# Kernel tuning notes

Hardware: AMD Instinct MI355X
Metric: run time of the kernel (lower is better)

Reference implementation:

```python
import jax, jax.numpy as jnp
import numpy as np

N_HEAD, D_HEAD, D_MODEL = 16, 64, 1024
QLEN, MLEN, BSZ = 512, 512, 8
KLEN = QLEN + MLEN
SCALE = 1.0 / D_HEAD ** 0.5
LN_EPS = 1e-5


def rel_shift(x):
    # x: [qlen, klen, bsz, n_head] -- Transformer-XL pad/reshape shift trick
    q, k, b, n = x.shape
    x_pad = jnp.pad(x, ((0, 0), (1, 0), (0, 0), (0, 0)))
    x_pad = x_pad.reshape(k + 1, q, b, n)
    return x_pad[1:].reshape(q, k, b, n)


def setup_inputs() -> dict:
    key = jax.random.key(0)
    ks = jax.random.split(key, 10)
    s = 0.02
    return {
        'w': jax.random.normal(ks[0], (QLEN, BSZ, D_MODEL), jnp.float32),
        'r': jax.random.normal(ks[1], (KLEN, D_MODEL), jnp.float32),
        'mems': jax.random.normal(ks[2], (MLEN, BSZ, D_MODEL), jnp.float32),
        'r_w_bias': jax.random.normal(ks[3], (N_HEAD, D_HEAD), jnp.float32) * s,
        'r_r_bias': jax.random.normal(ks[4], (N_HEAD, D_HEAD), jnp.float32) * s,
        'Wq': jax.random.normal(ks[5], (N_HEAD * D_HEAD, D_MODEL), jnp.float32) * s,
        'Wkv': jax.random.normal(ks[6], (2 * N_HEAD * D_HEAD, D_MODEL), jnp.float32) * s,
        'Wr': jax.random.normal(ks[7], (N_HEAD * D_HEAD, D_MODEL), jnp.float32) * s,
        'br': jnp.zeros((N_HEAD * D_HEAD,), jnp.float32),
        'Wo': jax.random.normal(ks[8], (D_MODEL, N_HEAD * D_HEAD), jnp.float32) * s,
        'bo': jnp.zeros((D_MODEL,), jnp.float32),
        'gamma': jnp.ones((D_MODEL,), jnp.float32),
        'beta': jnp.zeros((D_MODEL,), jnp.float32),
    }


def reference(w, r, mems, r_w_bias, r_r_bias, Wq, Wkv, Wr, br, Wo, bo, gamma, beta):
    qlen, bsz, _ = w.shape
    cat = jnp.concatenate([mems, w], axis=0)           # [klen, b, d]
    klen = cat.shape[0]
    mlen = klen - qlen

    q = (w @ Wq.T).reshape(qlen, bsz, N_HEAD, D_HEAD)   # [i, b, n, d]
    kv = (cat @ Wkv.T).reshape(klen, bsz, N_HEAD, 2 * D_HEAD)
    k, v = kv[..., :D_HEAD], kv[..., D_HEAD:]           # [j, b, n, d]
    rk = (r @ Wr.T + br).reshape(klen, N_HEAD, D_HEAD)  # [j, n, d]

    AC = jnp.einsum('ibnd,jbnd->ijbn', q + r_w_bias, k)
    BD = jnp.einsum('ibnd,jnd->ijbn', q + r_r_bias, rk)
    BD = rel_shift(BD)
    score = (AC + BD) * SCALE                           # [i, j, b, n]

    # causal mask with memory: query i attends to keys j <= i + mlen
    i_idx = jnp.arange(qlen)[:, None]
    j_idx = jnp.arange(klen)[None, :]
    mask = j_idx > (i_idx + mlen)
    score = jnp.where(mask[:, :, None, None], -1e30, score)

    prob = jax.nn.softmax(score, axis=1)
    attn_vec = jnp.einsum('ijbn,jbnd->ibnd', prob, v).reshape(qlen, bsz, N_HEAD * D_HEAD)
    attn_out = attn_vec @ Wo.T + bo

    # IdentityResidualGate: x + relu(y), then LayerNorm
    y = w + jax.nn.relu(attn_out)
    mu = jnp.mean(y, axis=-1, keepdims=True)
    var = jnp.mean(jnp.square(y - mu), axis=-1, keepdims=True)
    return (y - mu) * jax.lax.rsqrt(var + LN_EPS) * gamma + beta
```

## Files before the change

kernel.cpp:

```cpp
#include <hip/hip_runtime.h>
#include <hip/hip_bf16.h>
#include <cstdint>
#include <cstddef>

typedef __attribute__((ext_vector_type(4))) float f32x4;
typedef __attribute__((ext_vector_type(8))) short bf16x8;
using u16 = unsigned short;

#define SCLOG2E 0.18033688011112043f

__device__ __forceinline__ u16 f2b(float f) {
    union { float f; uint32_t u; } x; x.f = f;
    uint32_t r = x.u + 0x7fffu + ((x.u >> 16) & 1u);
    return (u16)(r >> 16);
}
__device__ __forceinline__ float b2f(u16 u) {
    union { uint32_t u; float f; } x; x.u = (uint32_t)u << 16; return x.f;
}

#define GLDS16(g, s)                                                        \
    __builtin_amdgcn_global_load_lds(                                       \
        (const __attribute__((address_space(1))) uint32_t*)(g),             \
        (__attribute__((address_space(3))) uint32_t*)(s), 16, 0, 0)

__global__ __launch_bounds__(256) void prep_kernel(
    const float* __restrict__ mems, const float* __restrict__ w,
    const float* __restrict__ r, const float* __restrict__ Wq,
    const float* __restrict__ Wkv, const float* __restrict__ Wr,
    const float* __restrict__ Wo, u16* __restrict__ cat_b,
    u16* __restrict__ r_b, u16* __restrict__ Wq_b, u16* __restrict__ Wkv_b,
    u16* __restrict__ Wr_b, u16* __restrict__ Wo_b) {
    int bid = blockIdx.x;
    if (bid < 8192) {
        int col4 = threadIdx.x;
        float4 v;
        int b, oj;
        if (bid < 4096) {
            v = reinterpret_cast<const float4*>(mems)[(size_t)bid * 256 + col4];
            b = bid & 7; oj = bid >> 3;
        } else {
            int rrow = bid - 4096;
            v = reinterpret_cast<const float4*>(w)[(size_t)rrow * 256 + col4];
            b = rrow & 7; oj = 512 + (rrow >> 3);
        }
        uint2 o;
        o.x = (uint32_t)f2b(v.x) | ((uint32_t)f2b(v.y) << 16);
        o.y = (uint32_t)f2b(v.z) | ((uint32_t)f2b(v.w) << 16);
        reinterpret_cast<uint2*>(cat_b)[(size_t)(b * 1024 + oj) * 256 + col4] = o;
        return;
    }
    bid -= 8192;
    const float4* src;
    uint2* dst;
    if (bid < 1024)      { src = (const float4*)r;   dst = (uint2*)r_b; }
    else if (bid < 2048) { src = (const float4*)Wq;  dst = (uint2*)Wq_b;  bid -= 1024; }
    else if (bid < 4096) { src = (const float4*)Wkv; dst = (uint2*)Wkv_b; bid -= 2048; }
    else if (bid < 5120) { src = (const float4*)Wr;  dst = (uint2*)Wr_b;  bid -= 4096; }
    else                 { src = (const float4*)Wo;  dst = (uint2*)Wo_b;  bid -= 5120; }
    int idx = bid * 256 + threadIdx.x;
    float4 v = src[idx];
    uint2 o;
    o.x = (uint32_t)f2b(v.x) | ((uint32_t)f2b(v.y) << 16);
    o.y = (uint32_t)f2b(v.z) | ((uint32_t)f2b(v.w) << 16);
    dst[idx] = o;
}

__global__ __launch_bounds__(512, 1) void kv_gemm(const u16* __restrict__ catb,
                                                  const u16* __restrict__ Wkvb,
                                                  u16* __restrict__ kb,
                                                  u16* __restrict__ vtb) {
    __shared__ u16 sA[2][256][64];
    __shared__ u16 sB[2][256][64];
    const int tid = threadIdx.x;
    const int wid = tid >> 6, lane = tid & 63;
    const int lr = lane & 15, lg = lane >> 4;
    const int bm = blockIdx.x * 256, bn = blockIdx.y * 256;
    const int Wm = (wid >> 2) * 128, Wn = (wid & 3) * 64;
    const int srow = tid >> 3, scol = tid & 7;
    const int xs = lr & 7;
    const u16* A = catb + (size_t)bm * 1024;
    const u16* B = Wkvb + (size_t)bn * 1024;
    f32x4 acc[8][4] = {};

#pragma unroll
    for (int p = 0; p < 4; p++) {
        int row = p * 64 + srow;
        int cs = (scol ^ (row & 7)) * 8;
        GLDS16(A + (size_t)row * 1024 + cs, &sA[0][row][scol * 8]);
        GLDS16(B + (size_t)row * 1024 + cs, &sB[0][row][scol * 8]);
    }
    __syncthreads();

    int cur = 0;
    for (int t = 0; t < 16; t++) {
        if (t < 15) {
            const int k0n = (t + 1) * 64;
#pragma unroll
            for (int p = 0; p < 4; p++) {
                int row = p * 64 + srow;
                int cs = (scol ^ (row & 7)) * 8;
                GLDS16(A + (size_t)row * 1024 + k0n + cs, &sA[cur ^ 1][row][scol * 8]);
                GLDS16(B + (size_t)row * 1024 + k0n + cs, &sB[cur ^ 1][row][scol * 8]);
            }
        }
#pragma unroll
        for (int ks = 0; ks < 2; ks++) {
            bf16x8 af[8], bfr[4];
#pragma unroll
            for (int mi = 0; mi < 8; mi++)
                af[mi] = *reinterpret_cast<const bf16x8*>(
                    &sA[cur][Wm + mi * 16 + lr][((ks * 4 + lg) ^ xs) * 8]);
#pragma unroll
            for (int ni = 0; ni < 4; ni++)
                bfr[ni] = *reinterpret_cast<const bf16x8*>(
                    &sB[cur][Wn + ni * 16 + lr][((ks * 4 + lg) ^ xs) * 8]);
#pragma unroll
            for (int mi = 0; mi < 8; mi++)
#pragma unroll
                for (int ni = 0; ni < 4; ni++)
                    acc[mi][ni] = __builtin_amdgcn_mfma_f32_16x16x32_bf16(
                        af[mi], bfr[ni], acc[mi][ni], 0, 0, 0);
        }
        __syncthreads();
        cur ^= 1;
    }
#pragma unroll
    for (int mi = 0; mi < 8; mi++)
#pragma unroll
        for (int ni = 0; ni < 4; ni++) {
            const int m0 = bm + Wm + mi * 16 + lg * 4;
            const int c = bn + Wn + ni * 16 + lr;
            const int b = m0 >> 10, j0 = m0 & 1023;
            const int n = c >> 7, dd = c & 127;
            if (dd < 64) {
#pragma unroll
                for (int rr = 0; rr < 4; rr++)
                    kb[(((size_t)(b * 16 + n)) * 1024 + j0 + rr) * 64 + dd] =
                        f2b(acc[mi][ni][rr]);
            } else {
                uint2 pk;
                pk.x = (uint32_t)f2b(acc[mi][ni][0]) | ((uint32_t)f2b(acc[mi][ni][1]) << 16);
                pk.y = (uint32_t)f2b(acc[mi][ni][2]) | ((uint32_t)f2b(acc[mi][ni][3]) << 16);
                *reinterpret_cast<uint2*>(
                    vtb + (((size_t)(b * 16 + n)) * 64 + (dd - 64)) * 1024 + j0) = pk;
            }
        }
}

__global__ __launch_bounds__(256, 2) void qr_gemm(
    const u16* __restrict__ catb, const u16* __restrict__ Wqb,
    const u16* __restrict__ rb, const u16* __restrict__ Wrb,
    const float* __restrict__ bw, const float* __restrict__ brr,
    const float* __restrict__ br, u16* __restrict__ qwb,
    u16* __restrict__ qrb, u16* __restrict__ rkb) {
    __shared__ u16 sA[2][128][64];
    __shared__ u16 sB[2][128][64];
    const int idx = blockIdx.x;
    const u16 *A, *B;
    int bx, by, epi;
    if (idx < 256) {
        epi = 0; B = Wqb; bx = idx & 31; by = idx >> 5;
        int bm0 = bx * 128;
        A = catb + ((size_t)(bm0 >> 9) * 1024 + 512 + (bm0 & 511)) * 1024;
    } else {
        epi = 2; B = Wrb;
        int l = idx - 256; bx = l & 7; by = l >> 3;
        A = rb + (size_t)bx * 128 * 1024;
    }
    const int tid = threadIdx.x;
    const int wid = tid >> 6, lane = tid & 63;
    const int lr = lane & 15, lg = lane >> 4;
    const int bm = bx * 128, bn = by * 128;
    const int wm = (wid >> 1) * 64, wn = (wid & 1) * 64;
    const int srow = tid >> 3, scol = tid & 7;
    f32x4 acc[4][4] = {};

#pragma unroll
    for (int p = 0; p < 4; p++) {
        int row = p * 32 + srow;
        GLDS16(A + (size_t)row * 1024 + scol * 8, &sA[0][row][scol * 8]);
        GLDS16(B + (size_t)(bn + row) * 1024 + scol * 8, &sB[0][row][scol * 8]);
    }
    __syncthreads();

    int cur = 0;
    for (int t = 0; t < 16; t++) {
        if (t < 15) {
            const int k0n = (t + 1) * 64;
#pragma unroll
            for (int p = 0; p < 4; p++) {
                int row = p * 32 + srow;
                GLDS16(A + (size_t)row * 1024 + k0n + scol * 8, &sA[cur ^ 1][row][scol * 8]);
                GLDS16(B + (size_t)(bn + row) * 1024 + k0n + scol * 8,
                       &sB[cur ^ 1][row][scol * 8]);
            }
        }
#pragma unroll
        for (int ks = 0; ks < 2; ks++) {
            bf16x8 af[4], bfr[4];
#pragma unroll
            for (int x = 0; x < 4; x++) {
                af[x] = *reinterpret_cast<const bf16x8*>(
                    &sA[cur][wm + x * 16 + lr][(ks * 4 + lg) * 8]);
                bfr[x] = *reinterpret_cast<const bf16x8*>(
                    &sB[cur][wn + x * 16 + lr][(ks * 4 + lg) * 8]);
            }
#pragma unroll
            for (int mi = 0; mi < 4; mi++)
#pragma unroll
                for (int ni = 0; ni < 4; ni++)
                    acc[mi][ni] = __builtin_amdgcn_mfma_f32_16x16x32_bf16(
                        af[mi], bfr[ni], acc[mi][ni], 0, 0, 0);
        }
        __syncthreads();
        cur ^= 1;
    }
#pragma unroll
    for (int mi = 0; mi < 4; mi++)
#pragma unroll
        for (int ni = 0; ni < 4; ni++) {
            const int m0 = bm + wm + mi * 16 + lg * 4;
            const int c = bn + wn + ni * 16 + lr;
            if (epi == 0) {
#pragma unroll
                for (int rr = 0; rr < 4; rr++) {
                    int m = m0 + rr;
                    qwb[(size_t)m * 1024 + c] = f2b((acc[mi][ni][rr] + bw[c]) * SCLOG2E);
                    qrb[(size_t)m * 1024 + c] = f2b((acc[mi][ni][rr] + brr[c]) * SCLOG2E);
                }
            } else {
                const int nh = c >> 6, d = c & 63;
#pragma unroll
                for (int rr = 0; rr < 4; rr++)
                    rkb[((size_t)nh * 1024 + m0 + rr) * 64 + d] = f2b(acc[mi][ni][rr] + br[c]);
            }
        }
}

__global__ __launch_bounds__(256, 2) void gemm_out(const u16* __restrict__ A,
                                                   const u16* __restrict__ B,
                                                   const float* __restrict__ wres,
                                                   const float* __restrict__ bo,
                                                   u16* __restrict__ y) {
    __shared__ u16 sA[2][128][64];
    __shared__ u16 sB[2][128][64];
    const int tid = threadIdx.x;
    const int wid = tid >> 6, lane = tid & 63;
    const int lr = lane & 15, lg = lane >> 4;
    const int bm = blockIdx.x * 128, bn = blockIdx.y * 128;
    const int wm = (wid >> 1) * 64, wn = (wid & 1) * 64;
    const int srow = tid >> 3, scol = tid & 7;
    f32x4 acc[4][4] = {};

#pragma unroll
    for (int p = 0; p < 4; p++) {
        int row = p * 32 + srow;
        GLDS16(A + (size_t)(bm + row) * 1024 + scol * 8, &sA[0][row][scol * 8]);
        GLDS16(B + (size_t)(bn + row) * 1024 + scol * 8, &sB[0][row][scol * 8]);
    }
    __syncthreads();

    int cur = 0;
    for (int t = 0; t < 16; t++) {
        if (t < 15) {
            const int k0n = (t + 1) * 64;
#pragma unroll
            for (int p = 0; p < 4; p++) {
                int row = p * 32 + srow;
                GLDS16(A + (size_t)(bm + row) * 1024 + k0n + scol * 8,
                       &sA[cur ^ 1][row][scol * 8]);
                GLDS16(B + (size_t)(bn + row) * 1024 + k0n + scol * 8,
                       &sB[cur ^ 1][row][scol * 8]);
            }
        }
#pragma unroll
        for (int ks = 0; ks < 2; ks++) {
            bf16x8 af[4], bfr[4];
#pragma unroll
            for (int x = 0; x < 4; x++) {
                af[x] = *reinterpret_cast<const bf16x8*>(
                    &sA[cur][wm + x * 16 + lr][(ks * 4 + lg) * 8]);
                bfr[x] = *reinterpret_cast<const bf16x8*>(
                    &sB[cur][wn + x * 16 + lr][(ks * 4 + lg) * 8]);
            }
#pragma unroll
            for (int mi = 0; mi < 4; mi++)
#pragma unroll
                for (int ni = 0; ni < 4; ni++)
                    acc[mi][ni] = __builtin_amdgcn_mfma_f32_16x16x32_bf16(
                        af[mi], bfr[ni], acc[mi][ni], 0, 0, 0);
        }
        __syncthreads();
        cur ^= 1;
    }
#pragma unroll
    for (int mi = 0; mi < 4; mi++)
#pragma unroll
        for (int ni = 0; ni < 4; ni++)
#pragma unroll
            for (int rr = 0; rr < 4; rr++) {
                int m = bm + wm + mi * 16 + lg * 4 + rr;
                int c = bn + wn + ni * 16 + lr;
                float v = wres[(size_t)m * 1024 + c] + fmaxf(acc[mi][ni][rr] + bo[c], 0.0f);
                y[(size_t)m * 1024 + c] = f2b(v);
            }
}

__global__ __launch_bounds__(512, 2) void attn_kernel(const u16* __restrict__ qw,
                                                      const u16* __restrict__ qr,
                                                      const u16* __restrict__ kbuf,
                                                      const u16* __restrict__ vt,
                                                      const u16* __restrict__ rkb,
                                                      u16* __restrict__ attnv) {
    __shared__ uint4 ksh[64][8];
    __shared__ uint4 vsh[64][8];
    __shared__ uint4 rsh[192][8];
    __shared__ u16 bds[8][16][82];
    __shared__ u16 ps[8][16][72];
    const int bid = blockIdx.x;
    const int wg = (bid & 7) * 64 + (bid >> 3);
    const int i0 = ((wg & 3) ^ 3) * 128;
    const int bnid = wg >> 2;
    const int b = bnid & 7, n = bnid >> 3;
    const int tid = threadIdx.x, wid = tid >> 6, lane = tid & 63;
    const int lr = lane & 15, lg = lane >> 4;
    const int it = i0 + wid * 16;

    const u16* qwp = qw + ((size_t)(b * 512 + it + lr)) * 1024 + n * 64;
    const u16* qrp = qr + ((size_t)(b * 512 + it + lr)) * 1024 + n * 64;
    bf16x8 aqw[2], aqr[2];
#pragma unroll
    for (int ks = 0; ks < 2; ks++) {
        aqw[ks] = *reinterpret_cast<const bf16x8*>(qwp + (ks * 4 + lg) * 8);
        aqr[ks] = *reinterpret_cast<const bf16x8*>(qrp + (ks * 4 + lg) * 8);
    }
    const u16* kp = kbuf + ((size_t)(b * 16 + n)) * 65536;
    const u16* vp = vt + ((size_t)(b * 16 + n)) * 65536;
    const u16* rp = rkb + (size_t)n * 65536;

    f32x4 acc[4] = {};
    float lpart[4] = {0.f, 0.f, 0.f, 0.f};
    const int xs = lr & 7;
    const int rbase = 112 - 16 * wid;
    const int jrb0 = 384 - i0;

#pragma unroll
    for (int p = 0; p < 2; p++) {
        int row = jrb0 + p * 64 + (tid >> 3);
        int c = tid & 7;
        int cp = ((jrb0 >> 6) + p) % 3;
        GLDS16(rp + (size_t)row * 64 + (c ^ (row & 7)) * 8,
               (char*)rsh + (size_t)(cp * 512 + wid * 64) * 16);
    }

    const int nt = (i0 + 703) >> 6;
    for (int t = 0; t < nt; t++) {
        const int j0 = t << 6;
        const int jrb = jrb0 + j0;
        {
            int row = tid >> 3, c = tid & 7;
            int cs = (c ^ (row & 7)) * 8;
            GLDS16(kp + (size_t)(j0 + row) * 64 + cs,
                   (char*)ksh + (size_t)(wid * 64) * 16);
            GLDS16(vp + (size_t)row * 1024 + j0 + cs,
                   (char*)vsh + (size_t)(wid * 64) * 16);
        }
        {
            int row = jrb + 128 + (tid >> 3);
            int c = tid & 7;
            int cw = ((jrb >> 6) + 2) % 3;
            int grow = row > 1023 ? 1023 : row;
            GLDS16(rp + (size_t)grow * 64 + (c ^ (row & 7)) * 8,
                   (char*)rsh + (size_t)(cw * 512 + wid * 64) * 16);
        }
        __syncthreads();

        __builtin_amdgcn_s_setprio(1);
        f32x4 s[4] = {};
#pragma unroll
        for (int fj = 0; fj < 4; fj++)
#pragma unroll
            for (int ks = 0; ks < 2; ks++) {
                bf16x8 bk = *reinterpret_cast<const bf16x8*>(
                    &ksh[fj * 16 + lr][(ks * 4 + lg) ^ xs]);
                s[fj] = __builtin_amdgcn_mfma_f32_16x16x32_bf16(aqw[ks], bk, s[fj], 0, 0, 0);
            }
        f32x4 bd[5] = {};
#pragma unroll
        for (int fb = 0; fb < 5; fb++) {
            int x = jrb + rbase + fb * 16;
            int slot = ((x >> 6) % 3) * 64 + (x & 63) + lr;
#pragma unroll
            for (int ks = 0; ks < 2; ks++) {
                bf16x8 brk = *reinterpret_cast<const bf16x8*>(
                    &rsh[slot][(ks * 4 + lg) ^ xs]);
                bd[fb] = __builtin_amdgcn_mfma_f32_16x16x32_bf16(aqr[ks], brk, bd[fb], 0, 0, 0);
            }
        }
        __builtin_amdgcn_s_setprio(0);
#pragma unroll
        for (int fb = 0; fb < 5; fb++)
#pragma unroll
            for (int rr = 0; rr < 4; rr++)
                bds[wid][lg * 4 + rr][fb * 16 + lr] = f2b(bd[fb][rr]);

#pragma unroll
        for (int fj = 0; fj < 4; fj++)
#pragma unroll
            for (int rr = 0; rr < 4; rr++) {
                const int di = lg * 4 + rr;
                float v = s[fj][rr] + b2f(bds[wid][di][fj * 16 + lr + 15 - di]);
                float e = (j0 + fj * 16 + lr <= it + di + 512) ? exp2f(v) : 0.0f;
                lpart[rr] += e;
                ps[wid][di][fj * 16 + lr] = f2b(e);
            }
        __builtin_amdgcn_s_setprio(1);
#pragma unroll
        for (int kc = 0; kc < 2; kc++) {
            bf16x8 ap = *reinterpret_cast<const bf16x8*>(&ps[wid][lr][kc * 32 + lg * 8]);
#pragma unroll
            for (int nd = 0; nd < 4; nd++) {
                bf16x8 bv = *reinterpret_cast<const bf16x8*>(
                    &vsh[nd * 16 + lr][(kc * 4 + lg) ^ xs]);
                acc[nd] = __builtin_amdgcn_mfma_f32_16x16x32_bf16(ap, bv, acc[nd], 0, 0, 0);
            }
        }
        __builtin_amdgcn_s_setprio(0);
        __syncthreads();
    }
    float l[4];
#pragma unroll
    for (int rr = 0; rr < 4; rr++) {
        float x = lpart[rr];
        x += __shfl_xor(x, 1);
        x += __shfl_xor(x, 2);
        x += __shfl_xor(x, 4);
        x += __shfl_xor(x, 8);
        l[rr] = x;
    }
#pragma unroll
    for (int nd = 0; nd < 4; nd++)
#pragma unroll
        for (int rr = 0; rr < 4; rr++) {
            int i = it + lg * 4 + rr;
            int d = nd * 16 + lr;
            attnv[((size_t)i * 8 + b) * 1024 + n * 64 + d] = f2b(acc[nd][rr] / l[rr]);
        }
}

__global__ __launch_bounds__(256) void ln_kernel(const u16* __restrict__ y,
                                                 const float* __restrict__ gamma,
                                                 const float* __restrict__ beta,
                                                 float* __restrict__ out) {
    __shared__ float rs[8];
    int row = blockIdx.x, tid = threadIdx.x;
    ushort4 u = reinterpret_cast<const ushort4*>(y + (size_t)row * 1024)[tid];
    float v0 = b2f(u.x), v1 = b2f(u.y), v2 = b2f(u.z), v3 = b2f(u.w);
    float s = v0 + v1 + v2 + v3;
    float s2 = v0 * v0 + v1 * v1 + v2 * v2 + v3 * v3;
#pragma unroll
    for (int m = 1; m < 64; m <<= 1) {
        s += __shfl_xor(s, m);
        s2 += __shfl_xor(s2, m);
    }
    if ((tid & 63) == 0) {
        rs[tid >> 6] = s;
        rs[4 + (tid >> 6)] = s2;
    }
    __syncthreads();
    s = rs[0] + rs[1] + rs[2] + rs[3];
    s2 = rs[4] + rs[5] + rs[6] + rs[7];
    float mu = s * (1.0f / 1024.0f);
    float var = s2 * (1.0f / 1024.0f) - mu * mu;
    float inv = rsqrtf(var + 1e-5f);
    float4 g = reinterpret_cast<const float4*>(gamma)[tid];
    float4 be = reinterpret_cast<const float4*>(beta)[tid];
    float4 o;
    o.x = (v0 - mu) * inv * g.x + be.x;
    o.y = (v1 - mu) * inv * g.y + be.y;
    o.z = (v2 - mu) * inv * g.z + be.z;
    o.w = (v3 - mu) * inv * g.w + be.w;
    reinterpret_cast<float4*>(out + (size_t)row * 1024)[tid] = o;
}

extern "C" void kernel_launch(void* const* d_in, const int* in_sizes, int n_in,
                              void* d_out, int out_size, void* d_ws, size_t ws_size,
                              hipStream_t stream) {
    (void)in_sizes; (void)n_in; (void)out_size; (void)ws_size;
    const float* w_in  = (const float*)d_in[0];
    const float* r_in  = (const float*)d_in[1];
    const float* mems  = (const float*)d_in[2];
    const float* bw    = (const float*)d_in[3];
    const float* brr   = (const float*)d_in[4];
    const float* Wq    = (const float*)d_in[5];
    const float* Wkv   = (const float*)d_in[6];
    const float* Wr    = (const float*)d_in[7];
    const float* br    = (const float*)d_in[8];
    const float* Wo    = (const float*)d_in[9];
    const float* bo    = (const float*)d_in[10];
    const float* gamma = (const float*)d_in[11];
    const float* beta  = (const float*)d_in[12];

    char* base = (char*)d_ws;
    size_t off = 0;
    auto alloc = [&](size_t bytes) -> char* {
        char* p = base + off;
        off += (bytes + 255) & ~(size_t)255;
        return p;
    };
    u16* cat_b = (u16*)alloc((size_t)8192 * 1024 * 2);
    u16* r_b   = (u16*)alloc((size_t)1024 * 1024 * 2);
    u16* Wq_b  = (u16*)alloc((size_t)1024 * 1024 * 2);
    u16* Wkv_b = (u16*)alloc((size_t)2048 * 1024 * 2);
    u16* Wr_b  = (u16*)alloc((size_t)1024 * 1024 * 2);
    u16* Wo_b  = (u16*)alloc((size_t)1024 * 1024 * 2);
    u16* qw_b  = (u16*)alloc((size_t)4096 * 1024 * 2);
    u16* qr_b  = (u16*)alloc((size_t)4096 * 1024 * 2);
    u16* k_b   = (u16*)alloc((size_t)128 * 1024 * 64 * 2);
    u16* vt_b  = (u16*)alloc((size_t)128 * 64 * 1024 * 2);
    u16* rk_b  = (u16*)alloc((size_t)16 * 1024 * 64 * 2);
    u16* av_b  = (u16*)alloc((size_t)4096 * 1024 * 2);
    u16* y     = (u16*)cat_b;

    prep_kernel<<<14336, 256, 0, stream>>>(mems, w_in, r_in, Wq, Wkv, Wr, Wo,
                                           cat_b, r_b, Wq_b, Wkv_b, Wr_b, Wo_b);

    kv_gemm<<<dim3(32, 8), 512, 0, stream>>>(cat_b, Wkv_b, k_b, vt_b);
    qr_gemm<<<320, 256, 0, stream>>>(cat_b, Wq_b, r_b, Wr_b, bw, brr, br,
                                     qw_b, qr_b, rk_b);

    attn_kernel<<<512, 512, 0, stream>>>(qw_b, qr_b, k_b, vt_b, rk_b, av_b);

    gemm_out<<<dim3(32, 8), 256, 0, stream>>>(av_b, Wo_b, w_in, bo, y);

    ln_kernel<<<4096, 256, 0, stream>>>(y, gamma, beta, (float*)d_out);
}
```

Baseline: 192.4 us.

## Prefetch next K/V/R tiles into registers to overlap loads with compute

Replaces the direct global-to-LDS loads issued at the top of each attention iteration with register prefetch of the next K, V and rel-position tiles. These are issued before the current tile's MFMA work and written to LDS after it. The first tiles and all three R ring slots are preloaded before the loop. The goal is to hide global load latency behind compute, at the cost of extra registers and two barriers per iteration instead of one.

```diff
diff --git a/kernel.cpp b/kernel.cpp
--- a/kernel.cpp
+++ b/kernel.cpp
@@ -344,36 +344,40 @@
     const int rbase = 112 - 16 * wid;
     const int jrb0 = 384 - i0;
 
-#pragma unroll
-    for (int p = 0; p < 2; p++) {
-        int row = jrb0 + p * 64 + (tid >> 3);
-        int c = tid & 7;
+    const int srow = tid >> 3, sc = tid & 7;
+
+    {
+        int cs = (sc ^ (srow & 7)) * 8;
+        GLDS16(kp + (size_t)srow * 64 + cs, (char*)ksh + (size_t)(wid * 64) * 16);
+        GLDS16(vp + (size_t)srow * 1024 + cs, (char*)vsh + (size_t)(wid * 64) * 16);
+    }
+#pragma unroll
+    for (int p = 0; p < 3; p++) {
+        int row = jrb0 + p * 64 + srow;
         int cp = ((jrb0 >> 6) + p) % 3;
-        GLDS16(rp + (size_t)row * 64 + (c ^ (row & 7)) * 8,
+        GLDS16(rp + (size_t)row * 64 + ((sc ^ (row & 7)) * 8),
                (char*)rsh + (size_t)(cp * 512 + wid * 64) * 16);
     }
+    __syncthreads();
 
     const int nt = (i0 + 703) >> 6;
     for (int t = 0; t < nt; t++) {
         const int j0 = t << 6;
         const int jrb = jrb0 + j0;
-        {
-            int row = tid >> 3, c = tid & 7;
-            int cs = (c ^ (row & 7)) * 8;
-            GLDS16(kp + (size_t)(j0 + row) * 64 + cs,
-                   (char*)ksh + (size_t)(wid * 64) * 16);
-            GLDS16(vp + (size_t)row * 1024 + j0 + cs,
-                   (char*)vsh + (size_t)(wid * 64) * 16);
-        }
-        {
-            int row = jrb + 128 + (tid >> 3);
-            int c = tid & 7;
-            int cw = ((jrb >> 6) + 2) % 3;
-            int grow = row > 1023 ? 1023 : row;
-            GLDS16(rp + (size_t)grow * 64 + (c ^ (row & 7)) * 8,
-                   (char*)rsh + (size_t)(cw * 512 + wid * 64) * 16);
-        }
-        __syncthreads();
+        const bool more = (t + 1 < nt);
+        uint4 kreg, vreg, rreg;
+        int rrow_u = 0;
+        if (more) {
+            const int j0n = j0 + 64;
+            kreg = *reinterpret_cast<const uint4*>(
+                kp + (size_t)(j0n + srow) * 64 + ((sc ^ (srow & 7)) * 8));
+            vreg = *reinterpret_cast<const uint4*>(
+                vp + (size_t)srow * 1024 + j0n + ((sc ^ (srow & 7)) * 8));
+            rrow_u = jrb + 192 + srow;
+            int grow = rrow_u > 1023 ? 1023 : rrow_u;
+            rreg = *reinterpret_cast<const uint4*>(
+                rp + (size_t)grow * 64 + ((sc ^ (rrow_u & 7)) * 8));
+        }
 
         __builtin_amdgcn_s_setprio(1);
         f32x4 s[4] = {};
@@ -426,7 +430,17 @@
             }
         }
         __builtin_amdgcn_s_setprio(0);
-        __syncthreads();
+
+        if (more) {
+            __syncthreads();
+            ksh[srow][sc] = kreg;
+            vsh[srow][sc] = vreg;
+            {
+                int cw = (jrb >> 6) % 3;
+                rsh[cw * 64 + (rrow_u & 63)][sc] = rreg;
+            }
+            __syncthreads();
+        }
     }
     float l[4];
 #pragma unroll
```

Measured after the change: 190.9 us. No clear change (-0.8%).
